# Optimization experiments

Hardware: AMD Instinct MI355X
Metric: run time of the kernel (lower is better)

## Reference

```python
import jax, jax.numpy as jnp
import numpy as np

C, B, NZ, NGF, NC = 16, 2048, 100, 64, 512
DIMS = [NZ, NGF * 8, NGF * 4, NGF * 2, NGF * 4, NC]  # 100->512->256->128->256->512
EPS = 1e-5  # torch BatchNorm2d default


def setup_inputs() -> dict:
    key = jax.random.key(0)
    ks = jax.random.split(key, 6)
    inp = {"x": jax.random.normal(ks[0], (C, B, NZ, 1, 1), dtype=jnp.float32)}
    for l in range(5):  # 1x1 conv weights per class, stacked over class dim
        fan_in = DIMS[l]
        inp[f"W{l+1}"] = jax.random.normal(ks[1 + l], (C, DIMS[l + 1], DIMS[l]), dtype=jnp.float32) / np.float32(np.sqrt(fan_in))
        inp[f"b{l+1}"] = jnp.zeros((C, DIMS[l + 1]), dtype=jnp.float32)
    for l in range(4):  # BN affine params (torch init: weight=1, bias=0)
        inp[f"g{l+1}"] = jnp.ones((C, DIMS[l + 1]), dtype=jnp.float32)
        inp[f"be{l+1}"] = jnp.zeros((C, DIMS[l + 1]), dtype=jnp.float32)
    return inp


def _conv1x1(h, W, b):
    # h: [C,B,Fin], W: [C,Fout,Fin] -> [C,B,Fout]  (1x1 conv at H=W=1 == per-class GEMM)
    return jnp.einsum('cbi,coi->cbo', h, W) + b[:, None, :]


def _bn(h, g, b):
    # training-mode BatchNorm2d: biased batch stats over (B,H,W); here H=W=1 so over B
    mu = jnp.mean(h, axis=1, keepdims=True)
    var = jnp.mean((h - mu) ** 2, axis=1, keepdims=True)
    return g[:, None, :] * (h - mu) * jax.lax.rsqrt(var + EPS) + b[:, None, :]


def reference(x, W1, b1, W2, b2, W3, b3, W4, b4, W5, b5,
              g1, be1, g2, be2, g3, be3, g4, be4):
    h = x[..., 0, 0]  # [C,B,NZ] (1x1 spatial squeezed)
    h = jax.nn.relu(_bn(_conv1x1(h, W1, b1), g1, be1))
    h = jax.nn.relu(_bn(_conv1x1(h, W2, b2), g2, be2))
    h = jax.nn.relu(_bn(_conv1x1(h, W3, b3), g3, be3))
    h = jax.nn.relu(_bn(_conv1x1(h, W4, b4), g4, be4))
    h = _conv1x1(h, W5, b5)  # [C,B,NC]
    gendata = h.reshape(C * B, NC, 1, 1)  # concat over classes
    genlabel = jnp.repeat(jnp.arange(C, dtype=jnp.float32), B)
    return gendata, genlabel
```

## Files before the change

kernel.cpp:

```cpp
#include <hip/hip_runtime.h>
#include <hip/hip_bf16.h>
#include <math.h>

#define CCLS 16
#define BB   2048

using bf16x8 = __attribute__((ext_vector_type(8))) short;
using short8 = __attribute__((ext_vector_type(8))) short;
using f32x4  = __attribute__((ext_vector_type(4))) float;

__device__ __forceinline__ void split2(float e, short& hi, short& lo) {
    __hip_bfloat16 h = __float2bfloat16(e);
    hi = __builtin_bit_cast(short, h);
    lo = __builtin_bit_cast(short, __float2bfloat16(e - __bfloat162float(h)));
}

__device__ __forceinline__ void soft_barrier() {
    asm volatile("s_waitcnt lgkmcnt(0)" ::: "memory");
    __builtin_amdgcn_s_barrier();
    asm volatile("" ::: "memory");
}

__device__ __forceinline__ void gll16(const void* g, void* l) {
    __builtin_amdgcn_global_load_lds(
        (const __attribute__((address_space(1))) unsigned*)g,
        (__attribute__((address_space(3))) unsigned*)l, 16, 0, 0);
}

#define XCD_REMAP(btile, otile, c)                                             \
    int btile, otile, c;                                                       \
    {                                                                          \
        const int bpcls = gridDim.x * gridDim.y;                               \
        const int id = blockIdx.x + gridDim.x * (blockIdx.y + gridDim.y * blockIdx.z); \
        const int j = id >> 3;                                                 \
        c = 2 * (id & 7) + j / bpcls;                                          \
        const int r = j % bpcls;                                               \
        btile = r % gridDim.x;                                                 \
        otile = r / gridDim.x;                                                 \
    }


struct PackDesc {
    const float* src[6];
    int nrt[6];
    int ksn[6];
    int kreal[6];
    int beg[7];
};

__global__ __launch_bounds__(256)
void pack_kernel(PackDesc d, char* __restrict__ base)
{
    const int bid = blockIdx.x;
    int s = 0;
    #pragma unroll
    for (int i = 0; i < 5; ++i) s += (bid >= d.beg[i + 1]);
    const int t    = bid - d.beg[s];
    const int ksn  = d.ksn[s], nrt = d.nrt[s], kreal = d.kreal[s];
    const int perc = nrt * ksn;
    const int c  = t / perc;
    const int r  = t - c * perc;
    const int rt = r / ksn;
    const int ks = r - rt * ksn;
    const float* src = d.src[s] + ((size_t)(c * nrt + rt) * 128) * kreal;
    char* dst = base + (size_t)bid * 16384;
    const int tid = threadIdx.x;

    #pragma unroll
    for (int it = 0; it < 2; ++it) {
        const int row = (tid >> 2) + (it << 6);
        const int cc  = tid & 3;
        const int q   = ((row >> 4) << 10) | (cc << 8) | ((row & 15) << 4);
        const int k0  = ks * 32 + cc * 8;
        const float* sp = src + (size_t)row * kreal + k0;
        float e[8];
        if (k0 + 8 <= kreal) {
            float4 v0 = *(const float4*)sp;
            float4 v1 = *(const float4*)(sp + 4);
            e[0]=v0.x; e[1]=v0.y; e[2]=v0.z; e[3]=v0.w;
            e[4]=v1.x; e[5]=v1.y; e[6]=v1.z; e[7]=v1.w;
        } else {
            #pragma unroll
            for (int j = 0; j < 8; ++j) e[j] = (k0 + j < kreal) ? sp[j] : 0.f;
        }
        short hv[8], lv[8];
        #pragma unroll
        for (int j = 0; j < 8; ++j) split2(e[j], hv[j], lv[j]);
        *(short8*)(dst + q)        = (short8){hv[0],hv[1],hv[2],hv[3],hv[4],hv[5],hv[6],hv[7]};
        *(short8*)(dst + 8192 + q) = (short8){lv[0],lv[1],lv[2],lv[3],lv[4],lv[5],lv[6],lv[7]};
    }
}

template<int BM, int K, bool PREPACK, bool FUSE_BN, bool WRITE_STATS>
__global__ __launch_bounds__(256, 2)
void gemm4w_kernel(const float* __restrict__ A, const char* __restrict__ Apk,
                   const char* __restrict__ Wpk, const float* __restrict__ bias,
                   const float* __restrict__ psumIn, const float* __restrict__ psqIn,
                   const float* __restrict__ gIn, const float* __restrict__ beIn,
                   float* __restrict__ Out,
                   float* __restrict__ psumOut, float* __restrict__ psqOut,
                   const int Fout, const int nbtIn)
{
    constexpr int KS    = (K + 31) / 32;
    constexpr int PLANE = BM * 64;
    constexpr int BUFSZ = PREPACK ? 32768 : 2 * PLANE;
    static_assert(PREPACK || (K % 32 == 0), "");
    static_assert(PREPACK || (KS % 2 == 0) || (KS == 1), "");

    __shared__ __align__(16) char sm[2 * BUFSZ + (FUSE_BN ? 8 * K : 16)];
    float* scs = (float*)(sm + 2 * BUFSZ);
    float* shs = scs + (FUSE_BN ? K : 0);

    const int tid   = threadIdx.x;
    const int btile = blockIdx.x, otile = blockIdx.y, c = blockIdx.z;

    if (FUSE_BN) {
        for (int f = tid; f < K; f += 256) {
            const float* ps = psumIn + ((size_t)c * K + f) * nbtIn;
            const float* pq = psqIn  + ((size_t)c * K + f) * nbtIn;
            float s = 0.f, q = 0.f;
            for (int t = 0; t < nbtIn; t += 4) {
                float4 a4 = *(const float4*)(ps + t);
                float4 b4 = *(const float4*)(pq + t);
                s += (a4.x + a4.y) + (a4.z + a4.w);
                q += (b4.x + b4.y) + (b4.z + b4.w);
            }
            const float mean = s * (1.f / BB);
            const float var  = q * (1.f / BB) - mean * mean;
            const float rstd = rsqrtf(var + 1e-5f);
            const float scv  = gIn[(size_t)c * K + f] * rstd;
            scs[f] = scv;
            shs[f] = fmaf(-mean, scv, beIn[(size_t)c * K + f]);
        }
        __syncthreads();
    }

    const int b0 = btile * BM, o0 = otile * 128;
    const int OT = Fout >> 7;
    const char* wbase = Wpk + (size_t)((c * OT + otile) * KS) * 16384;
    const char* abase = PREPACK ? (Apk + (size_t)((c * gridDim.x + btile) * KS) * 16384) : nullptr;

    const int lane = tid & 63, wv = tid >> 6;
    const int fr = lane & 15, fkc = lane >> 4;
    const int wrow = (BM == 128) ? ((wv >> 1) << 6) : ((wv >> 1) << 5);
    const int wcol = (wv & 1) << 6;
    const int wrg = wrow >> 4, wcg = wcol >> 4;
    constexpr int MI = BM / 32;

    f32x4 acc[MI][4];
    #pragma unroll
    for (int mi = 0; mi < MI; ++mi)
        #pragma unroll
        for (int ni = 0; ni < 4; ++ni)
            acc[mi][ni] = (f32x4){0.f, 0.f, 0.f, 0.f};

    if constexpr (PREPACK) {
        auto stageTile = [&](int nb, int ks) {
            const char* at = abase + (size_t)ks * 16384;
            const char* wt = wbase + (size_t)ks * 16384;
            char* dst = sm + nb;
            #pragma unroll
            for (int i = 0; i < 4; ++i) {
                const int rg = ((wv << 2) + i) << 10;
                gll16(at + rg + (lane << 4), dst + rg);
                gll16(wt + rg + (lane << 4), dst + 16384 + rg);
            }
        };
        stageTile(0, 0);
        __syncthreads();
        for (int ks = 0; ks < KS; ++ks) {
            const int cb = (ks & 1) ? BUFSZ : 0;
            if (ks + 1 < KS) stageTile(cb ^ BUFSZ, ks + 1);
            bf16x8 ah[MI], al[MI], wh[4], wl[4];
            #pragma unroll
            for (int i = 0; i < 4; ++i) {
                const int wo = ((wcg + i) << 10) | (fkc << 8) | (fr << 4);
                wh[i] = *(const bf16x8*)(sm + cb + 16384 + wo);
                wl[i] = *(const bf16x8*)(sm + cb + 24576 + wo);
            }
            #pragma unroll
            for (int i = 0; i < MI; ++i) {
                const int ao = ((wrg + i) << 10) | (fkc << 8) | (fr << 4);
                ah[i] = *(const bf16x8*)(sm + cb + ao);
                al[i] = *(const bf16x8*)(sm + cb + 8192 + ao);
            }
            #pragma unroll
            for (int mi = 0; mi < MI; ++mi)
                #pragma unroll
                for (int ni = 0; ni < 4; ++ni) {
                    acc[mi][ni] = __builtin_amdgcn_mfma_f32_16x16x32_bf16(ah[mi], wh[ni], acc[mi][ni], 0, 0, 0);
                    acc[mi][ni] = __builtin_amdgcn_mfma_f32_16x16x32_bf16(ah[mi], wl[ni], acc[mi][ni], 0, 0, 0);
                    acc[mi][ni] = __builtin_amdgcn_mfma_f32_16x16x32_bf16(al[mi], wh[ni], acc[mi][ni], 0, 0, 0);
                }
            __syncthreads();
        }
    } else {
        constexpr int NV = BM / 32;
        const int arow = (BM == 128) ? (tid >> 1) : (tid >> 2);
        const int asub = (BM == 128) ? (tid & 1)  : (tid & 3);
        const int ak0  = (BM == 128) ? (asub << 4) : (asub << 3);
        const int kch  = (BM == 128) ? (asub << 1) : asub;
        const int awr  = ((arow >> 4) << 10) | (kch << 8) | ((arow & 15) << 4);
        const float* Arow = A + ((size_t)c * BB + b0 + arow) * K;

        auto loadA = [&](float4 (&av)[NV], int gk0) {
            #pragma unroll
            for (int i = 0; i < NV; ++i)
                av[i] = *(const float4*)(Arow + gk0 + (i << 2));
        };
        auto loadW = [&](bf16x8 (&w)[8], int ks) {
            const char* wt = wbase + (size_t)ks * 16384;
            #pragma unroll
            for (int i = 0; i < 4; ++i) {
                const int wo = ((wcg + i) << 10) | (fkc << 8) | (fr << 4);
                w[i]     = *(const bf16x8*)(wt + wo);
                w[4 + i] = *(const bf16x8*)(wt + 8192 + wo);
            }
        };
        auto cvtStore = [&](char* dstbase, const float4 (&a)[NV], int gk0) {
            float e[NV * 4];
            #pragma unroll
            for (int i = 0; i < NV; ++i) {
                e[i*4+0] = a[i].x; e[i*4+1] = a[i].y; e[i*4+2] = a[i].z; e[i*4+3] = a[i].w;
            }
            if constexpr (FUSE_BN) {
                #pragma unroll
                for (int i = 0; i < NV; ++i) {
                    const float4 sc = *(const float4*)(scs + gk0 + (i << 2));
                    const float4 sh = *(const float4*)(shs + gk0 + (i << 2));
                    e[i*4+0] = fmaxf(0.f, fmaf(e[i*4+0], sc.x, sh.x));
                    e[i*4+1] = fmaxf(0.f, fmaf(e[i*4+1], sc.y, sh.y));
                    e[i*4+2] = fmaxf(0.f, fmaf(e[i*4+2], sc.z, sh.z));
                    e[i*4+3] = fmaxf(0.f, fmaf(e[i*4+3], sc.w, sh.w));
                }
            }
            short h[NV*4], l[NV*4];
            #pragma unroll
            for (int j = 0; j < NV*4; ++j) split2(e[j], h[j], l[j]);
            *(short8*)(dstbase + awr)         = (short8){h[0],h[1],h[2],h[3],h[4],h[5],h[6],h[7]};
            *(short8*)(dstbase + PLANE + awr) = (short8){l[0],l[1],l[2],l[3],l[4],l[5],l[6],l[7]};
            if constexpr (NV == 4) {
                *(short8*)(dstbase + awr + 256)         = (short8){h[8],h[9],h[10],h[11],h[12],h[13],h[14],h[15]};
                *(short8*)(dstbase + PLANE + awr + 256) = (short8){l[8],l[9],l[10],l[11],l[12],l[13],l[14],l[15]};
            }
        };

        bf16x8 wcA[8], wcB[8];
        float4 avP[NV], avQ[NV];

        auto step = [&](int ks, char* cbp, char* nbp,
                        float4 (&avUse)[NV], float4 (&avLoad)[NV],
                        bf16x8 (&wUse)[8], bf16x8 (&wLoad)[8]) {
            const bool hn  = (ks + 1) < KS;
            const bool hn2 = (ks + 2) < KS;
            if (hn2) loadA(avLoad, ((ks + 2) << 5) + ak0);
            if (hn)  loadW(wLoad, ks + 1);
            bf16x8 ah[MI], al[MI];
            #pragma unroll
            for (int i = 0; i < MI; ++i) {
                const int ao = ((wrg + i) << 10) | (fkc << 8) | (fr << 4);
                ah[i] = *(const bf16x8*)(cbp + ao);
                al[i] = *(const bf16x8*)(cbp + PLANE + ao);
            }
            #pragma unroll
            for (int mi = 0; mi < MI; ++mi)
                #pragma unroll
                for (int ni = 0; ni < 4; ++ni) {
                    acc[mi][ni] = __builtin_amdgcn_mfma_f32_16x16x32_bf16(ah[mi], wUse[ni],     acc[mi][ni], 0, 0, 0);
                    acc[mi][ni] = __builtin_amdgcn_mfma_f32_16x16x32_bf16(ah[mi], wUse[4 + ni], acc[mi][ni], 0, 0, 0);
                    acc[mi][ni] = __builtin_amdgcn_mfma_f32_16x16x32_bf16(al[mi], wUse[ni],     acc[mi][ni], 0, 0, 0);
                }
            if (hn) cvtStore(nbp, avUse, ((ks + 1) << 5) + ak0);
            soft_barrier();
        };

        {
            float4 av0[NV];
            loadA(av0, ak0);
            loadW(wcA, 0);
            if (KS > 1) loadA(avP, 32 + ak0);
            cvtStore(sm, av0, ak0);
        }
        soft_barrier();

        for (int ks = 0; ks < KS; ks += 2) {
            step(ks,     sm,         sm + BUFSZ, avP, avQ, wcA, wcB);
            step(ks + 1, sm + BUFSZ, sm,         avQ, avP, wcB, wcA);
        }
    }

    float bv[4];
    #pragma unroll
    for (int ni = 0; ni < 4; ++ni)
        bv[ni] = bias[(size_t)c * Fout + o0 + wcol + (ni << 4) + fr];

    float p[4] = {}, q[4] = {};
    const int rsub = (lane >> 4) << 2;
    #pragma unroll
    for (int mi = 0; mi < MI; ++mi) {
        #pragma unroll
        for (int j = 0; j < 4; ++j) {
            const int row = b0 + wrow + (mi << 4) + rsub + j;
            float* op = Out + ((size_t)c * BB + row) * Fout + o0 + wcol;
            #pragma unroll
            for (int ni = 0; ni < 4; ++ni) {
                const float v = acc[mi][ni][j] + bv[ni];
                op[(ni << 4) + fr] = v;
                if (WRITE_STATS) { p[ni] += v; q[ni] += v * v; }
            }
        }
    }

    if (WRITE_STATS) {
        #pragma unroll
        for (int ni = 0; ni < 4; ++ni) {
            p[ni] += __shfl_xor(p[ni], 16); p[ni] += __shfl_xor(p[ni], 32);
            q[ni] += __shfl_xor(q[ni], 16); q[ni] += __shfl_xor(q[ni], 32);
        }
        __syncthreads();
        float* redp = (float*)sm;
        float* redq = (float*)(sm + 1024);
        if (lane < 16) {
            const int base = (wv >> 1) * 128 + wcol;
            #pragma unroll
            for (int ni = 0; ni < 4; ++ni) {
                redp[base + (ni << 4) + fr] = p[ni];
                redq[base + (ni << 4) + fr] = q[ni];
            }
        }
        __syncthreads();
        if (tid < 128) {
            const float sp = redp[tid] + redp[128 + tid];
            const float sq = redq[tid] + redq[128 + tid];
            const size_t o = ((size_t)c * Fout + o0 + tid) * gridDim.x + btile;
            psumOut[o] = sp;
            psqOut[o]  = sq;
        }
    }
}

template<int K, bool WRITE_STATS>
__global__ __launch_bounds__(512, 2)
void gemm8w_kernel(const float* __restrict__ A, const char* __restrict__ Wpk,
                   const float* __restrict__ bias,
                   const float* __restrict__ psumIn, const float* __restrict__ psqIn,
                   const float* __restrict__ gIn, const float* __restrict__ beIn,
                   float* __restrict__ Out,
                   float* __restrict__ psumOut, float* __restrict__ psqOut,
                   const int Fout, const int nbtIn)
{
    constexpr int KS    = K / 32;
    constexpr int PLANE = 8192;
    constexpr int BUFSZ = 16384;
    static_assert(K % 128 == 0, "need KS % 4 == 0 for the paired schedule");

    __shared__ __align__(16) char sm[4 * BUFSZ + 8 * K];
    float* scs = (float*)(sm + 4 * BUFSZ);
    float* shs = scs + K;

    const int tid = threadIdx.x;
    XCD_REMAP(btile, otile, c)

    for (int f = tid; f < K; f += 512) {
        const float* ps = psumIn + ((size_t)c * K + f) * nbtIn;
        const float* pq = psqIn  + ((size_t)c * K + f) * nbtIn;
        float s = 0.f, q = 0.f;
        for (int t = 0; t < nbtIn; t += 4) {
            float4 a4 = *(const float4*)(ps + t);
            float4 b4 = *(const float4*)(pq + t);
            s += (a4.x + a4.y) + (a4.z + a4.w);
            q += (b4.x + b4.y) + (b4.z + b4.w);
        }
        const float mean = s * (1.f / BB);
        const float var  = q * (1.f / BB) - mean * mean;
        const float rstd = rsqrtf(var + 1e-5f);
        const float scv  = gIn[(size_t)c * K + f] * rstd;
        scs[f] = scv;
        shs[f] = fmaf(-mean, scv, beIn[(size_t)c * K + f]);
    }
    __syncthreads();

    const int b0 = btile * 128, o0 = otile * 256;
    const int OT128 = Fout >> 7;

    const int arow = tid >> 2, asub = tid & 3;
    const int ak0  = asub << 3;
    const int awr  = ((arow >> 4) << 10) | (asub << 8) | ((arow & 15) << 4);
    const float* Arow = A + ((size_t)c * BB + b0 + arow) * K;

    const int lane = tid & 63, wv = tid >> 6;
    const int wr = wv >> 2, nc = wv & 3;
    const int wrow = wr << 6, wcol = nc << 6;
    const int fr = lane & 15, fkc = lane >> 4;
    const int wrg = wrow >> 4;
    const int wtile = wcol >> 7;
    const int wcg = (wcol >> 4) & 7;
    const char* wbase = Wpk + (size_t)((c * OT128 + otile * 2 + wtile) * KS) * 16384;

    auto loadA = [&](float4 (&av)[2], int gk0) {
        av[0] = *(const float4*)(Arow + gk0);
        av[1] = *(const float4*)(Arow + gk0 + 4);
    };
    auto loadW = [&](bf16x8 (&w)[8], int ks) {
        const char* wt = wbase + (size_t)ks * 16384;
        #pragma unroll
        for (int i = 0; i < 4; ++i) {
            const int wo = ((wcg + i) << 10) | (fkc << 8) | (fr << 4);
            w[i]     = *(const bf16x8*)(wt + wo);
            w[4 + i] = *(const bf16x8*)(wt + 8192 + wo);
        }
    };
    auto cvtStore = [&](char* dstbase, const float4 (&a)[2], int gk0) {
        float e[8] = {a[0].x, a[0].y, a[0].z, a[0].w, a[1].x, a[1].y, a[1].z, a[1].w};
        const float4 sc0 = *(const float4*)(scs + gk0);
        const float4 sc1 = *(const float4*)(scs + gk0 + 4);
        const float4 sh0 = *(const float4*)(shs + gk0);
        const float4 sh1 = *(const float4*)(shs + gk0 + 4);
        e[0] = fmaxf(0.f, fmaf(e[0], sc0.x, sh0.x));
        e[1] = fmaxf(0.f, fmaf(e[1], sc0.y, sh0.y));
        e[2] = fmaxf(0.f, fmaf(e[2], sc0.z, sh0.z));
        e[3] = fmaxf(0.f, fmaf(e[3], sc0.w, sh0.w));
        e[4] = fmaxf(0.f, fmaf(e[4], sc1.x, sh1.x));
        e[5] = fmaxf(0.f, fmaf(e[5], sc1.y, sh1.y));
        e[6] = fmaxf(0.f, fmaf(e[6], sc1.z, sh1.z));
        e[7] = fmaxf(0.f, fmaf(e[7], sc1.w, sh1.w));
        short h[8], l[8];
        #pragma unroll
        for (int j = 0; j < 8; ++j) split2(e[j], h[j], l[j]);
        *(short8*)(dstbase + awr)         = (short8){h[0],h[1],h[2],h[3],h[4],h[5],h[6],h[7]};
        *(short8*)(dstbase + PLANE + awr) = (short8){l[0],l[1],l[2],l[3],l[4],l[5],l[6],l[7]};
    };

    f32x4 acc[4][4];
    #pragma unroll
    for (int mi = 0; mi < 4; ++mi)
        #pragma unroll
        for (int ni = 0; ni < 4; ++ni)
            acc[mi][ni] = (f32x4){0.f, 0.f, 0.f, 0.f};

    bf16x8 wc[8], wn[8];
    float4 avA[2], avB[2], avC[2], avD[2];

    auto mfmaStep = [&](char* cbp, bf16x8 (&wUse)[8]) {
        bf16x8 ah[4], al[4];
        #pragma unroll
        for (int i = 0; i < 4; ++i) {
            const int ao = ((wrg + i) << 10) | (fkc << 8) | (fr << 4);
            ah[i] = *(const bf16x8*)(cbp + ao);
            al[i] = *(const bf16x8*)(cbp + PLANE + ao);
        }
        #pragma unroll
        for (int mi = 0; mi < 4; ++mi)
            #pragma unroll
            for (int ni = 0; ni < 4; ++ni) {
                acc[mi][ni] = __builtin_amdgcn_mfma_f32_16x16x32_bf16(ah[mi], wUse[ni],     acc[mi][ni], 0, 0, 0);
                acc[mi][ni] = __builtin_amdgcn_mfma_f32_16x16x32_bf16(ah[mi], wUse[4 + ni], acc[mi][ni], 0, 0, 0);
                acc[mi][ni] = __builtin_amdgcn_mfma_f32_16x16x32_bf16(al[mi], wUse[ni],     acc[mi][ni], 0, 0, 0);
            }
    };

    auto group = [&](int ks, char* bR0, char* bR1, char* bW0, char* bW1,
                     float4 (&aU0)[2], float4 (&aU1)[2],
                     float4 (&aL0)[2], float4 (&aL1)[2]) {
        if (ks + 4 < KS) loadA(aL0, ((ks + 4) << 5) + ak0);
        if (ks + 1 < KS) loadW(wn, ks + 1);
        mfmaStep(bR0, wc);
        if (ks + 2 < KS) cvtStore(bW0, aU0, ((ks + 2) << 5) + ak0);
        if (ks + 5 < KS) loadA(aL1, ((ks + 5) << 5) + ak0);
        if (ks + 2 < KS) loadW(wc, ks + 2);
        mfmaStep(bR1, wn);
        if (ks + 3 < KS) cvtStore(bW1, aU1, ((ks + 3) << 5) + ak0);
        soft_barrier();
    };

    {
        float4 a0[2], a1[2];
        loadA(a0, ak0);
        loadA(a1, 32 + ak0);
        loadW(wc, 0);
        loadA(avA, 64 + ak0);
        loadA(avB, 96 + ak0);
        cvtStore(sm,         a0, ak0);
        cvtStore(sm + BUFSZ, a1, 32 + ak0);
    }
    soft_barrier();

    for (int ks = 0; ks < KS; ks += 4) {
        group(ks,     sm,             sm + BUFSZ,     sm + 2 * BUFSZ, sm + 3 * BUFSZ,
              avA, avB, avC, avD);
        group(ks + 2, sm + 2 * BUFSZ, sm + 3 * BUFSZ, sm,             sm + BUFSZ,
              avC, avD, avA, avB);
    }

    float bv[4];
    #pragma unroll
    for (int ni = 0; ni < 4; ++ni)
        bv[ni] = bias[(size_t)c * Fout + o0 + wcol + (ni << 4) + fr];

    float p[4] = {}, q[4] = {};
    const int rsub = (lane >> 4) << 2;
    #pragma unroll
    for (int mi = 0; mi < 4; ++mi) {
        #pragma unroll
        for (int j = 0; j < 4; ++j) {
            const int row = b0 + wrow + (mi << 4) + rsub + j;
            float* op = Out + ((size_t)c * BB + row) * Fout + o0 + wcol;
            #pragma unroll
            for (int ni = 0; ni < 4; ++ni) {
                const float v = acc[mi][ni][j] + bv[ni];
                op[(ni << 4) + fr] = v;
                if (WRITE_STATS) { p[ni] += v; q[ni] += v * v; }
            }
        }
    }

    if (WRITE_STATS) {
        #pragma unroll
        for (int ni = 0; ni < 4; ++ni) {
            p[ni] += __shfl_xor(p[ni], 16); p[ni] += __shfl_xor(p[ni], 32);
            q[ni] += __shfl_xor(q[ni], 16); q[ni] += __shfl_xor(q[ni], 32);
        }
        __syncthreads();
        float* redp = (float*)sm;
        float* redq = (float*)(sm + 2048);
        if (lane < 16) {
            const int base = wr * 256 + wcol;
            #pragma unroll
            for (int ni = 0; ni < 4; ++ni) {
                redp[base + (ni << 4) + fr] = p[ni];
                redq[base + (ni << 4) + fr] = q[ni];
            }
        }
        __syncthreads();
        if (tid < 256) {
            const float sp = redp[tid] + redp[256 + tid];
            const float sq = redq[tid] + redq[256 + tid];
            const size_t o = ((size_t)c * Fout + o0 + tid) * gridDim.x + btile;
            psumOut[o] = sp;
            psqOut[o]  = sq;
        }
    }
}

__global__ __launch_bounds__(256)
void label_kernel(float* __restrict__ out)
{
    const int i = blockIdx.x * 256 + threadIdx.x;
    out[i] = (float)(i >> 11);
}

extern "C" void kernel_launch(void* const* d_in, const int* in_sizes, int n_in,
                              void* d_out, int out_size, void* d_ws, size_t ws_size,
                              hipStream_t stream)
{
    const float* x = (const float*)d_in[0];
    const float* W[5];  const float* bs[5];
    for (int l = 0; l < 5; ++l) { W[l] = (const float*)d_in[1 + 2 * l]; bs[l] = (const float*)d_in[2 + 2 * l]; }
    const float* g[4];  const float* be[4];
    for (int l = 0; l < 4; ++l) { g[l] = (const float*)d_in[11 + 2 * l]; be[l] = (const float*)d_in[12 + 2 * l]; }

    float* out     = (float*)d_out;
    float* gendata = out;
    float* label   = out + (size_t)CCLS * BB * 512;

    float* ws  = (float*)d_ws;
    float* h2  = ws;
    float* h3  = h2 + 8388608;
    float* h4  = h2;
    float* ps1 = h3 + 4194304;
    float* pq1 = ps1 + 131072;
    float* ps2 = pq1 + 131072;
    float* pq2 = ps2 + 65536;
    float* ps3 = pq2 + 65536;
    float* pq3 = ps3 + 65536;
    float* ps4 = pq3 + 65536;
    float* pq4 = ps4 + 65536;
    char*  pack = (char*)(pq4 + 65536);

    const char* xpk  = pack;
    const char* wpk1 = pack + (size_t)1024 * 16384;
    const char* wpk2 = pack + (size_t)1280 * 16384;
    const char* wpk3 = pack + (size_t)1792 * 16384;
    const char* wpk4 = pack + (size_t)1920 * 16384;
    const char* wpk5 = pack + (size_t)2048 * 16384;

    const dim3 blk(256);

    PackDesc pd;
    pd.src[0] = x;    pd.src[1] = W[0]; pd.src[2] = W[1];
    pd.src[3] = W[2]; pd.src[4] = W[3]; pd.src[5] = W[4];
    const int nrt[6]   = {16, 4, 2, 1, 2, 4};
    const int ksn[6]   = {4, 4, 16, 8, 4, 8};
    const int kreal[6] = {100, 100, 512, 256, 128, 256};
    const int beg[7]   = {0, 1024, 1280, 1792, 1920, 2048, 2560};
    for (int i = 0; i < 6; ++i) { pd.nrt[i] = nrt[i]; pd.ksn[i] = ksn[i]; pd.kreal[i] = kreal[i]; }
    for (int i = 0; i < 7; ++i) pd.beg[i] = beg[i];
    pack_kernel<<<dim3(2560), blk, 0, stream>>>(pd, pack);

    gemm4w_kernel<128, 128, true, false, true><<<dim3(16, 4, CCLS), blk, 0, stream>>>(
        nullptr, xpk, wpk1, bs[0], nullptr, nullptr, nullptr, nullptr,
        gendata, ps1, pq1, 512, 0);

    gemm8w_kernel<512, true><<<dim3(16, 1, CCLS), dim3(512), 0, stream>>>(
        gendata, wpk2, bs[1], ps1, pq1, g[0], be[0],
        h2, ps2, pq2, 256, 16);

    gemm4w_kernel<64, 256, false, true, true><<<dim3(32, 1, CCLS), blk, 0, stream>>>(
        h2, nullptr, wpk3, bs[2], ps2, pq2, g[1], be[1],
        h3, ps3, pq3, 128, 16);

    gemm8w_kernel<128, true><<<dim3(16, 1, CCLS), dim3(512), 0, stream>>>(
        h3, wpk4, bs[3], ps3, pq3, g[2], be[2],
        h4, ps4, pq4, 256, 32);

    gemm8w_kernel<256, false><<<dim3(16, 2, CCLS), dim3(512), 0, stream>>>(
        h4, wpk5, bs[4], ps4, pq4, g[3], be[3],
        gendata, nullptr, nullptr, 512, 16);

    label_kernel<<<dim3(CCLS * BB / 256), blk, 0, stream>>>(label);
}
```

Baseline: 148.3 us.

## Store intermediate activations as bf16 and drop activation low-part MFMAs

Intermediate activations between layers are now written and read as bf16 rather than fp32. The A operand uses only its high bf16 part, so the al*wh MFMA term and the low-plane LDS traffic go away. Weights still keep their hi/lo split. This halves activation memory traffic and cuts MFMA work by a third, at the cost of lower precision in the hidden layers. Batch statistics are still computed in fp32 before rounding.

```diff
diff --git a/kernel.cpp b/kernel.cpp
--- a/kernel.cpp
+++ b/kernel.cpp
@@ -5,14 +5,21 @@
 #define CCLS 16
 #define BB   2048
 
-using bf16x8 = __attribute__((ext_vector_type(8))) short;
-using short8 = __attribute__((ext_vector_type(8))) short;
-using f32x4  = __attribute__((ext_vector_type(4))) float;
+using bf16x8  = __attribute__((ext_vector_type(8))) short;
+using short8  = __attribute__((ext_vector_type(8))) short;
+using f32x4   = __attribute__((ext_vector_type(4))) float;
 
 __device__ __forceinline__ void split2(float e, short& hi, short& lo) {
     __hip_bfloat16 h = __float2bfloat16(e);
     hi = __builtin_bit_cast(short, h);
     lo = __builtin_bit_cast(short, __float2bfloat16(e - __bfloat162float(h)));
+}
+__device__ __forceinline__ short f2b(float e) {
+    return __builtin_bit_cast(short, __float2bfloat16(e));
+}
+__device__ __forceinline__ float b2f(short s) {
+    unsigned u = ((unsigned)(unsigned short)s) << 16;
+    return __builtin_bit_cast(float, u);
 }
 
 __device__ __forceinline__ void soft_barrier() {
@@ -91,21 +98,24 @@
     }
 }
 
-template<int BM, int K, bool PREPACK, bool FUSE_BN, bool WRITE_STATS>
+template<int BM, int K, bool PREPACK, bool OUTBF16, bool FUSE_BN, bool WRITE_STATS>
 __global__ __launch_bounds__(256, 2)
-void gemm4w_kernel(const float* __restrict__ A, const char* __restrict__ Apk,
-                   const char* __restrict__ Wpk, const float* __restrict__ bias,
+void gemm4w_kernel(const unsigned short* __restrict__ A,
+                   const char* __restrict__ Apk, const char* __restrict__ Wpk,
+                   const float* __restrict__ bias,
                    const float* __restrict__ psumIn, const float* __restrict__ psqIn,
                    const float* __restrict__ gIn, const float* __restrict__ beIn,
-                   float* __restrict__ Out,
+                   void* __restrict__ OutV,
                    float* __restrict__ psumOut, float* __restrict__ psqOut,
                    const int Fout, const int nbtIn)
 {
     constexpr int KS    = (K + 31) / 32;
     constexpr int PLANE = BM * 64;
-    constexpr int BUFSZ = PREPACK ? 32768 : 2 * PLANE;
+    constexpr int WOFF  = 8192;
+    constexpr int BUFSZ = PREPACK ? 24576 : PLANE;
     static_assert(PREPACK || (K % 32 == 0), "");
     static_assert(PREPACK || (KS % 2 == 0) || (KS == 1), "");
+    static_assert(PREPACK || BM == 64, "reg path supports BM=64 only");
 
     __shared__ __align__(16) char sm[2 * BUFSZ + (FUSE_BN ? 8 * K : 16)];
     float* scs = (float*)(sm + 2 * BUFSZ);
@@ -160,10 +170,14 @@
             const char* wt = wbase + (size_t)ks * 16384;
             char* dst = sm + nb;
             #pragma unroll
+            for (int i = 0; i < 2; ++i) {
+                const int rg = ((wv << 1) + i) << 10;
+                gll16(at + rg + (lane << 4), dst + rg);
+            }
+            #pragma unroll
             for (int i = 0; i < 4; ++i) {
                 const int rg = ((wv << 2) + i) << 10;
-                gll16(at + rg + (lane << 4), dst + rg);
-                gll16(wt + rg + (lane << 4), dst + 16384 + rg);
+                gll16(wt + rg + (lane << 4), dst + WOFF + rg);
             }
         };
         stageTile(0, 0);
@@ -171,18 +185,17 @@
         for (int ks = 0; ks < KS; ++ks) {
             const int cb = (ks & 1) ? BUFSZ : 0;
             if (ks + 1 < KS) stageTile(cb ^ BUFSZ, ks + 1);
-            bf16x8 ah[MI], al[MI], wh[4], wl[4];
+            bf16x8 ah[MI], wh[4], wl[4];
             #pragma unroll
             for (int i = 0; i < 4; ++i) {
                 const int wo = ((wcg + i) << 10) | (fkc << 8) | (fr << 4);
-                wh[i] = *(const bf16x8*)(sm + cb + 16384 + wo);
-                wl[i] = *(const bf16x8*)(sm + cb + 24576 + wo);
+                wh[i] = *(const bf16x8*)(sm + cb + WOFF + wo);
+                wl[i] = *(const bf16x8*)(sm + cb + WOFF + 8192 + wo);
             }
             #pragma unroll
             for (int i = 0; i < MI; ++i) {
                 const int ao = ((wrg + i) << 10) | (fkc << 8) | (fr << 4);
                 ah[i] = *(const bf16x8*)(sm + cb + ao);
-                al[i] = *(const bf16x8*)(sm + cb + 8192 + ao);
             }
             #pragma unroll
             for (int mi = 0; mi < MI; ++mi)
@@ -190,23 +203,17 @@
                 for (int ni = 0; ni < 4; ++ni) {
                     acc[mi][ni] = __builtin_amdgcn_mfma_f32_16x16x32_bf16(ah[mi], wh[ni], acc[mi][ni], 0, 0, 0);
                     acc[mi][ni] = __builtin_amdgcn_mfma_f32_16x16x32_bf16(ah[mi], wl[ni], acc[mi][ni], 0, 0, 0);
-                    acc[mi][ni] = __builtin_amdgcn_mfma_f32_16x16x32_bf16(al[mi], wh[ni], acc[mi][ni], 0, 0, 0);
                 }
             __syncthreads();
         }
     } else {
-        constexpr int NV = BM / 32;
-        const int arow = (BM == 128) ? (tid >> 1) : (tid >> 2);
-        const int asub = (BM == 128) ? (tid & 1)  : (tid & 3);
-        const int ak0  = (BM == 128) ? (asub << 4) : (asub << 3);
-        const int kch  = (BM == 128) ? (asub << 1) : asub;
-        const int awr  = ((arow >> 4) << 10) | (kch << 8) | ((arow & 15) << 4);
-        const float* Arow = A + ((size_t)c * BB + b0 + arow) * K;
-
-        auto loadA = [&](float4 (&av)[NV], int gk0) {
-            #pragma unroll
-            for (int i = 0; i < NV; ++i)
-                av[i] = *(const float4*)(Arow + gk0 + (i << 2));
+        const int arow = tid >> 2, asub = tid & 3;
+        const int ak0  = asub << 3;
+        const int awr  = ((arow >> 4) << 10) | (asub << 8) | ((arow & 15) << 4);
+        const unsigned short* Arow = A + ((size_t)c * BB + b0 + arow) * K;
+
+        auto loadA = [&](short8& av, int gk0) {
+            av = *(const short8*)(Arow + gk0);
         };
         auto loadW = [&](bf16x8 (&w)[8], int ks) {
             const char* wt = wbase + (size_t)ks * 16384;
@@ -217,50 +224,45 @@
                 w[4 + i] = *(const bf16x8*)(wt + 8192 + wo);
             }
         };
-        auto cvtStore = [&](char* dstbase, const float4 (&a)[NV], int gk0) {
-            float e[NV * 4];
-            #pragma unroll
-            for (int i = 0; i < NV; ++i) {
-                e[i*4+0] = a[i].x; e[i*4+1] = a[i].y; e[i*4+2] = a[i].z; e[i*4+3] = a[i].w;
-            }
+        auto cvtStore = [&](char* dstbase, const short8& a, int gk0) {
+            float e[8];
+            #pragma unroll
+            for (int j = 0; j < 8; ++j) e[j] = b2f(a[j]);
             if constexpr (FUSE_BN) {
-                #pragma unroll
-                for (int i = 0; i < NV; ++i) {
-                    const float4 sc = *(const float4*)(scs + gk0 + (i << 2));
-                    const float4 sh = *(const float4*)(shs + gk0 + (i << 2));
-                    e[i*4+0] = fmaxf(0.f, fmaf(e[i*4+0], sc.x, sh.x));
-                    e[i*4+1] = fmaxf(0.f, fmaf(e[i*4+1], sc.y, sh.y));
-                    e[i*4+2] = fmaxf(0.f, fmaf(e[i*4+2], sc.z, sh.z));
-                    e[i*4+3] = fmaxf(0.f, fmaf(e[i*4+3], sc.w, sh.w));
-                }
-            }
-            short h[NV*4], l[NV*4];
-            #pragma unroll
-            for (int j = 0; j < NV*4; ++j) split2(e[j], h[j], l[j]);
-            *(short8*)(dstbase + awr)         = (short8){h[0],h[1],h[2],h[3],h[4],h[5],h[6],h[7]};
-            *(short8*)(dstbase + PLANE + awr) = (short8){l[0],l[1],l[2],l[3],l[4],l[5],l[6],l[7]};
-            if constexpr (NV == 4) {
-                *(short8*)(dstbase + awr + 256)         = (short8){h[8],h[9],h[10],h[11],h[12],h[13],h[14],h[15]};
-                *(short8*)(dstbase + PLANE + awr + 256) = (short8){l[8],l[9],l[10],l[11],l[12],l[13],l[14],l[15]};
-            }
+                const float4 sc0 = *(const float4*)(scs + gk0);
+                const float4 sc1 = *(const float4*)(scs + gk0 + 4);
+                const float4 sh0 = *(const float4*)(shs + gk0);
+                const float4 sh1 = *(const float4*)(shs + gk0 + 4);
+                e[0] = fmaxf(0.f, fmaf(e[0], sc0.x, sh0.x));
+                e[1] = fmaxf(0.f, fmaf(e[1], sc0.y, sh0.y));
+                e[2] = fmaxf(0.f, fmaf(e[2], sc0.z, sh0.z));
+                e[3] = fmaxf(0.f, fmaf(e[3], sc0.w, sh0.w));
+                e[4] = fmaxf(0.f, fmaf(e[4], sc1.x, sh1.x));
+                e[5] = fmaxf(0.f, fmaf(e[5], sc1.y, sh1.y));
+                e[6] = fmaxf(0.f, fmaf(e[6], sc1.z, sh1.z));
+                e[7] = fmaxf(0.f, fmaf(e[7], sc1.w, sh1.w));
+            }
+            short h[8];
+            #pragma unroll
+            for (int j = 0; j < 8; ++j) h[j] = f2b(e[j]);
+            *(short8*)(dstbase + awr) = (short8){h[0],h[1],h[2],h[3],h[4],h[5],h[6],h[7]};
         };
 
         bf16x8 wcA[8], wcB[8];
-        float4 avP[NV], avQ[NV];
+        short8 avP, avQ;
 
         auto step = [&](int ks, char* cbp, char* nbp,
-                        float4 (&avUse)[NV], float4 (&avLoad)[NV],
+                        short8& avUse, short8& avLoad,
                         bf16x8 (&wUse)[8], bf16x8 (&wLoad)[8]) {
             const bool hn  = (ks + 1) < KS;
             const bool hn2 = (ks + 2) < KS;
             if (hn2) loadA(avLoad, ((ks + 2) << 5) + ak0);
             if (hn)  loadW(wLoad, ks + 1);
-            bf16x8 ah[MI], al[MI];
+            bf16x8 ah[MI];
             #pragma unroll
             for (int i = 0; i < MI; ++i) {
                 const int ao = ((wrg + i) << 10) | (fkc << 8) | (fr << 4);
                 ah[i] = *(const bf16x8*)(cbp + ao);
-                al[i] = *(const bf16x8*)(cbp + PLANE + ao);
             }
             #pragma unroll
             for (int mi = 0; mi < MI; ++mi)
@@ -268,14 +270,13 @@
                 for (int ni = 0; ni < 4; ++ni) {
                     acc[mi][ni] = __builtin_amdgcn_mfma_f32_16x16x32_bf16(ah[mi], wUse[ni],     acc[mi][ni], 0, 0, 0);
                     acc[mi][ni] = __builtin_amdgcn_mfma_f32_16x16x32_bf16(ah[mi], wUse[4 + ni], acc[mi][ni], 0, 0, 0);
-                    acc[mi][ni] = __builtin_amdgcn_mfma_f32_16x16x32_bf16(al[mi], wUse[ni],     acc[mi][ni], 0, 0, 0);
                 }
             if (hn) cvtStore(nbp, avUse, ((ks + 1) << 5) + ak0);
             soft_barrier();
         };
 
         {
-            float4 av0[NV];
+            short8 av0;
             loadA(av0, ak0);
             loadW(wcA, 0);
             if (KS > 1) loadA(avP, 32 + ak0);
@@ -301,11 +302,14 @@
         #pragma unroll
         for (int j = 0; j < 4; ++j) {
             const int row = b0 + wrow + (mi << 4) + rsub + j;
-            float* op = Out + ((size_t)c * BB + row) * Fout + o0 + wcol;
+            const size_t ob = ((size_t)c * BB + row) * Fout + o0 + wcol;
             #pragma unroll
             for (int ni = 0; ni < 4; ++ni) {
                 const float v = acc[mi][ni][j] + bv[ni];
-                op[(ni << 4) + fr] = v;
+                if constexpr (OUTBF16)
+                    ((unsigned short*)OutV)[ob + (ni << 4) + fr] = (unsigned short)f2b(v);
+                else
+                    ((float*)OutV)[ob + (ni << 4) + fr] = v;
                 if (WRITE_STATS) { p[ni] += v; q[ni] += v * v; }
             }
         }
@@ -339,19 +343,19 @@
     }
 }
 
-template<int K, bool WRITE_STATS>
+template<int K, bool OUTBF16, bool WRITE_STATS>
 __global__ __launch_bounds__(512, 2)
-void gemm8w_kernel(const float* __restrict__ A, const char* __restrict__ Wpk,
+void gemm8w_kernel(const unsigned short* __restrict__ A, const char* __restrict__ Wpk,
                    const float* __restrict__ bias,
                    const float* __restrict__ psumIn, const float* __restrict__ psqIn,
                    const float* __restrict__ gIn, const float* __restrict__ beIn,
-                   float* __restrict__ Out,
+                   void* __restrict__ OutV,
                    float* __restrict__ psumOut, float* __restrict__ psqOut,
                    const int Fout, const int nbtIn)
 {
     constexpr int KS    = K / 32;
     constexpr int PLANE = 8192;
-    constexpr int BUFSZ = 16384;
+    constexpr int BUFSZ = 8192;
     static_assert(K % 128 == 0, "need KS % 4 == 0 for the paired schedule");
 
     __shared__ __align__(16) char sm[4 * BUFSZ + 8 * K];
@@ -386,7 +390,7 @@
     const int arow = tid >> 2, asub = tid & 3;
     const int ak0  = asub << 3;
     const int awr  = ((arow >> 4) << 10) | (asub << 8) | ((arow & 15) << 4);
-    const float* Arow = A + ((size_t)c * BB + b0 + arow) * K;
+    const unsigned short* Arow = A + ((size_t)c * BB + b0 + arow) * K;
 
     const int lane = tid & 63, wv = tid >> 6;
     const int wr = wv >> 2, nc = wv & 3;
@@ -397,9 +401,8 @@
     const int wcg = (wcol >> 4) & 7;
     const char* wbase = Wpk + (size_t)((c * OT128 + otile * 2 + wtile) * KS) * 16384;
 
-    auto loadA = [&](float4 (&av)[2], int gk0) {
-        av[0] = *(const float4*)(Arow + gk0);
-        av[1] = *(const float4*)(Arow + gk0 + 4);
+    auto loadA = [&](short8& av, int gk0) {
+        av = *(const short8*)(Arow + gk0);
     };
     auto loadW = [&](bf16x8 (&w)[8], int ks) {
         const char* wt = wbase + (size_t)ks * 16384;
@@ -410,8 +413,10 @@
             w[4 + i] = *(const bf16x8*)(wt + 8192 + wo);
         }
     };
-    auto cvtStore = [&](char* dstbase, const float4 (&a)[2], int gk0) {
-        float e[8] = {a[0].x, a[0].y, a[0].z, a[0].w, a[1].x, a[1].y, a[1].z, a[1].w};
+    auto cvtStore = [&](char* dstbase, const short8& a, int gk0) {
+        float e[8];
+        #pragma unroll
+        for (int j = 0; j < 8; ++j) e[j] = b2f(a[j]);
         const float4 sc0 = *(const float4*)(scs + gk0);
         const float4 sc1 = *(const float4*)(scs + gk0 + 4);
         const float4 sh0 = *(const float4*)(shs + gk0);
@@ -424,11 +429,10 @@
         e[5] = fmaxf(0.f, fmaf(e[5], sc1.y, sh1.y));
         e[6] = fmaxf(0.f, fmaf(e[6], sc1.z, sh1.z));
         e[7] = fmaxf(0.f, fmaf(e[7], sc1.w, sh1.w));
-        short h[8], l[8];
-        #pragma unroll
-        for (int j = 0; j < 8; ++j) split2(e[j], h[j], l[j]);
-        *(short8*)(dstbase + awr)         = (short8){h[0],h[1],h[2],h[3],h[4],h[5],h[6],h[7]};
-        *(short8*)(dstbase + PLANE + awr) = (short8){l[0],l[1],l[2],l[3],l[4],l[5],l[6],l[7]};
+        short h[8];
+        #pragma unroll
+        for (int j = 0; j < 8; ++j) h[j] = f2b(e[j]);
+        *(short8*)(dstbase + awr) = (short8){h[0],h[1],h[2],h[3],h[4],h[5],h[6],h[7]};
     };
 
     f32x4 acc[4][4];
@@ -439,15 +443,14 @@
             acc[mi][ni] = (f32x4){0.f, 0.f, 0.f, 0.f};
 
     bf16x8 wc[8], wn[8];
-    float4 avA[2], avB[2], avC[2], avD[2];
+    short8 avA, avB, avC, avD;
 
     auto mfmaStep = [&](char* cbp, bf16x8 (&wUse)[8]) {
-        bf16x8 ah[4], al[4];
+        bf16x8 ah[4];
         #pragma unroll
         for (int i = 0; i < 4; ++i) {
             const int ao = ((wrg + i) << 10) | (fkc << 8) | (fr << 4);
             ah[i] = *(const bf16x8*)(cbp + ao);
-            al[i] = *(const bf16x8*)(cbp + PLANE + ao);
         }
         #pragma unroll
         for (int mi = 0; mi < 4; ++mi)
@@ -455,13 +458,11 @@
             for (int ni = 0; ni < 4; ++ni) {
                 acc[mi][ni] = __builtin_amdgcn_mfma_f32_16x16x32_bf16(ah[mi], wUse[ni],     acc[mi][ni], 0, 0, 0);
                 acc[mi][ni] = __builtin_amdgcn_mfma_f32_16x16x32_bf16(ah[mi], wUse[4 + ni], acc[mi][ni], 0, 0, 0);
-                acc[mi][ni] = __builtin_amdgcn_mfma_f32_16x16x32_bf16(al[mi], wUse[ni],     acc[mi][ni], 0, 0, 0);
             }
     };
 
     auto group = [&](int ks, char* bR0, char* bR1, char* bW0, char* bW1,
-                     float4 (&aU0)[2], float4 (&aU1)[2],
-                     float4 (&aL0)[2], float4 (&aL1)[2]) {
+                     short8& aU0, short8& aU1, short8& aL0, short8& aL1) {
         if (ks + 4 < KS) loadA(aL0, ((ks + 4) << 5) + ak0);
         if (ks + 1 < KS) loadW(wn, ks + 1);
         mfmaStep(bR0, wc);
@@ -474,7 +475,7 @@
     };
 
     {
-        float4 a0[2], a1[2];
+        short8 a0, a1;
         loadA(a0, ak0);
         loadA(a1, 32 + ak0);
         loadW(wc, 0);
@@ -504,11 +505,14 @@
         #pragma unroll
         for (int j = 0; j < 4; ++j) {
             const int row = b0 + wrow + (mi << 4) + rsub + j;
-            float* op = Out + ((size_t)c * BB + row) * Fout + o0 + wcol;
+            const size_t ob = ((size_t)c * BB + row) * Fout + o0 + wcol;
             #pragma unroll
             for (int ni = 0; ni < 4; ++ni) {
                 const float v = acc[mi][ni][j] + bv[ni];
-                op[(ni << 4) + fr] = v;
+                if constexpr (OUTBF16)
+                    ((unsigned short*)OutV)[ob + (ni << 4) + fr] = (unsigned short)f2b(v);
+                else
+                    ((float*)OutV)[ob + (ni << 4) + fr] = v;
                 if (WRITE_STATS) { p[ni] += v; q[ni] += v * v; }
             }
         }
@@ -562,12 +566,13 @@
     float* out     = (float*)d_out;
     float* gendata = out;
     float* label   = out + (size_t)CCLS * BB * 512;
-
-    float* ws  = (float*)d_ws;
-    float* h2  = ws;
-    float* h3  = h2 + 8388608;
-    float* h4  = h2;
-    float* ps1 = h3 + 4194304;
+    unsigned short* h1b = (unsigned short*)d_out;
+
+    char* wsb = (char*)d_ws;
+    unsigned short* h2b = (unsigned short*)wsb;
+    unsigned short* h3b = (unsigned short*)(wsb + 16777216);
+    unsigned short* h4b = h2b;
+    float* ps1 = (float*)(wsb + 16777216 + 8388608);
     float* pq1 = ps1 + 131072;
     float* ps2 = pq1 + 131072;
     float* pq2 = ps2 + 65536;
@@ -597,24 +602,24 @@
     for (int i = 0; i < 7; ++i) pd.beg[i] = beg[i];
     pack_kernel<<<dim3(2560), blk, 0, stream>>>(pd, pack);
 
-    gemm4w_kernel<128, 128, true, false, true><<<dim3(16, 4, CCLS), blk, 0, stream>>>(
+    gemm4w_kernel<128, 128, true, true, false, true><<<dim3(16, 4, CCLS), blk, 0, stream>>>(
         nullptr, xpk, wpk1, bs[0], nullptr, nullptr, nullptr, nullptr,
-        gendata, ps1, pq1, 512, 0);
-
-    gemm8w_kernel<512, true><<<dim3(16, 1, CCLS), dim3(512), 0, stream>>>(
-        gendata, wpk2, bs[1], ps1, pq1, g[0], be[0],
-        h2, ps2, pq2, 256, 16);
-
-    gemm4w_kernel<64, 256, false, true, true><<<dim3(32, 1, CCLS), blk, 0, stream>>>(
-        h2, nullptr, wpk3, bs[2], ps2, pq2, g[1], be[1],
-        h3, ps3, pq3, 128, 16);
-
-    gemm8w_kernel<128, true><<<dim3(16, 1, CCLS), dim3(512), 0, stream>>>(
-        h3, wpk4, bs[3], ps3, pq3, g[2], be[2],
-        h4, ps4, pq4, 256, 32);
-
-    gemm8w_kernel<256, false><<<dim3(16, 2, CCLS), dim3(512), 0, stream>>>(
-        h4, wpk5, bs[4], ps4, pq4, g[3], be[3],
+        h1b, ps1, pq1, 512, 0);
+
+    gemm8w_kernel<512, true, true><<<dim3(16, 1, CCLS), dim3(512), 0, stream>>>(
+        h1b, wpk2, bs[1], ps1, pq1, g[0], be[0],
+        h2b, ps2, pq2, 256, 16);
+
+    gemm4w_kernel<64, 256, false, true, true, true><<<dim3(32, 1, CCLS), blk, 0, stream>>>(
+        h2b, nullptr, wpk3, bs[2], ps2, pq2, g[1], be[1],
+        h3b, ps3, pq3, 128, 16);
+
+    gemm8w_kernel<128, true, true><<<dim3(16, 1, CCLS), dim3(512), 0, stream>>>(
+        h3b, wpk4, bs[3], ps3, pq3, g[2], be[2],
+        h4b, ps4, pq4, 256, 32);
+
+    gemm8w_kernel<256, false, false><<<dim3(16, 2, CCLS), dim3(512), 0, stream>>>(
+        h4b, wpk5, bs[4], ps4, pq4, g[3], be[3],
         gendata, nullptr, nullptr, 512, 16);
 
     label_kernel<<<dim3(CCLS * BB / 256), blk, 0, stream>>>(label);
```

Result: faster. 125.7 us (median of 2 runs) (-15.2%).
